# Optimization experiments

Hardware: AMD Instinct MI355X
Metric: run time of the kernel (lower is better)

## Reference

```python
import jax, jax.numpy as jnp
import numpy as np

B = 32768
IN_FULL = 3 * 32 * 32   # 3072 flattened
IN_DIM = 1024           # capped input dim
EMBED = 16
TINY = 16               # max(16, hidden_dim//4) with hidden_dim=32
OUT = 1000
NE = 4


def setup_inputs() -> dict:
    key = jax.random.key(0)
    ks = jax.random.split(key, 10)
    s = 0.05
    return {
        "x": jax.random.normal(ks[0], (B, 3, 32, 32), dtype=jnp.float32),
        "W_embed": jax.random.normal(ks[1], (EMBED, IN_DIM), dtype=jnp.float32) * s,
        "b_embed": jax.random.normal(ks[2], (EMBED,), dtype=jnp.float32) * s,
        "W1": jax.random.normal(ks[3], (NE, EMBED, TINY), dtype=jnp.float32) * s,
        "b1": jax.random.normal(ks[4], (NE, TINY), dtype=jnp.float32) * s,
        "W2": jax.random.normal(ks[5], (NE, TINY, OUT), dtype=jnp.float32) * s,
        "b2": jax.random.normal(ks[6], (NE, OUT), dtype=jnp.float32) * s,
        "Wg": jax.random.normal(ks[7], (NE, EMBED), dtype=jnp.float32) * s,
        "bg": jax.random.normal(ks[8], (NE,), dtype=jnp.float32) * s,
    }


def reference(x, W_embed, b_embed, W1, b1, W2, b2, Wg, bg):
    # flatten and truncate to input_dim (torch: x.view(B,-1)[:, :1024])
    xf = x.reshape(x.shape[0], -1)[:, :IN_DIM]
    # shared embedding: relu(Linear)
    e = jax.nn.relu(xf @ W_embed.T + b_embed)              # [B, EMBED]
    # gate: softmax(Linear)
    gate = jax.nn.softmax(e @ Wg.T + bg, axis=-1)          # [B, NE]
    # all 4 experts batched: relu(fc1) -> fc2 (dropout is eval-mode identity)
    h = jax.nn.relu(jnp.einsum('bd,edh->beh', e, W1) + b1[None])   # [B, NE, TINY]
    eo = jnp.einsum('beh,eho->beo', h, W2) + b2[None]              # [B, NE, OUT]
    # gate-weighted sum over experts
    out = jnp.einsum('beo,be->bo', eo, gate)               # [B, OUT]
    return out
```

## Files before the change

### kernel.cpp

```cpp
#include <hip/hip_runtime.h>
#include <cstddef>
#include <cstdint>

typedef short short8 __attribute__((ext_vector_type(8)));
typedef float floatx4 __attribute__((ext_vector_type(4)));

#define BATCH   32768
#define IN_DIM  1024
#define ROW_F   3072
#define EMBED   16
#define TINY    16
#define OUT     1000
#define NE      4
#define KPAD    96
#define NT_N    63

#define HW_BYTES ((size_t)BATCH * KPAD * 2)
#define BF_BYTES ((size_t)NT_N * 3 * 64 * 8 * 2)
#define WEF_SHORTS (32 * 64 * 8 * 2)

__device__ __forceinline__ unsigned short f2bf_rne(float f) {
    unsigned u = __builtin_bit_cast(unsigned, f);
    return (unsigned short)((u + 0x7FFFu + ((u >> 16) & 1u)) >> 16);
}

__global__ void k_prep(const float* __restrict__ W2, const float* __restrict__ b2,
                       const float* __restrict__ W_embed,
                       unsigned short* __restrict__ Bf,
                       unsigned short* __restrict__ WeF) {
    int tid = blockIdx.x * 256 + threadIdx.x;
    if (blockIdx.x < 48) {
        if (tid >= NT_N * 3 * 64) return;
        int n = tid / 192, r = tid % 192, s = r / 64, lane = r % 64;
        int col = n * 16 + (lane & 15);
        int kq = s * 32 + (lane >> 4) * 8;
        #pragma unroll
        for (int i = 0; i < 8; ++i) {
            int k = kq + i;
            float v = 0.f;
            if (col < OUT) {
                if (k < 64) v = W2[(size_t)((k >> 4) * 16 + (k & 15)) * OUT + col];
                else if (k < 68) v = b2[(size_t)(k - 64) * OUT + col];
            }
            Bf[(size_t)tid * 8 + i] = f2bf_rne(v);
        }
    } else {
        int id = tid - 48 * 256;
        if (id >= 32 * 64) return;
        int s = id >> 6, lane = id & 63;
        int j = lane & 15;
        int kq = s * 32 + ((lane >> 4) << 3);
        #pragma unroll
        for (int i = 0; i < 8; ++i) {
            float w = W_embed[(size_t)j * IN_DIM + kq + i];
            unsigned u = __builtin_bit_cast(unsigned, w);
            WeF[id * 8 + i] = (unsigned short)(u >> 16);
            float hif = __builtin_bit_cast(float, u & 0xFFFF0000u);
            float d = w - hif;
            WeF[16384 + id * 8 + i] =
                (unsigned short)(__builtin_bit_cast(unsigned, d) >> 16);
        }
    }
}

__global__ __launch_bounds__(256, 2) void k_embed(
    const float* __restrict__ x, const unsigned short* __restrict__ WeF,
    const float* __restrict__ b_embed, const float* __restrict__ W1,
    const float* __restrict__ b1, const float* __restrict__ Wg,
    const float* __restrict__ bg, unsigned short* __restrict__ hw)
{
    __shared__ short bb_lds[WEF_SHORTS];
    __shared__ float e_lds[4][16 * 20];
    __shared__ float g_lds[4][64];

    const int tid = threadIdx.x;
    {
        const float4* src = (const float4*)WeF;
        float4* dst = (float4*)bb_lds;
        #pragma unroll
        for (int i = 0; i < 16; ++i)
            dst[tid + i * 256] = src[tid + i * 256];
    }
    __syncthreads();

    const int lane = tid & 63;
    const int wv   = tid >> 6;
    const int quad = lane >> 4;
    const int jcol = lane & 15;
    const int tile = blockIdx.x * 4 + wv;
    const int row0 = tile * 16;

    const float be  = b_embed[jcol];
    const float bgr = bg[quad];
    float wgr[EMBED], w1r[EMBED];
    #pragma unroll
    for (int j = 0; j < EMBED; ++j) {
        wgr[j] = Wg[quad * EMBED + j];
        w1r[j] = W1[(size_t)(quad * EMBED + j) * TINY + jcol];
    }
    const float b1r = b1[lane];

    const short8* bhv = (const short8*)bb_lds;
    const short8* blv = (const short8*)(bb_lds + 16384);

    const float* xrow = x + (size_t)(row0 + jcol) * ROW_F + quad * 8;

    floatx4 acc0 = {0, 0, 0, 0}, acc1 = {0, 0, 0, 0};

    auto step = [&](float4 A0, float4 A1, int s) {
        float fa[8] = {A0.x, A0.y, A0.z, A0.w, A1.x, A1.y, A1.z, A1.w};
        short8 ahi, alo;
        #pragma unroll
        for (int m = 0; m < 8; ++m) {
            unsigned u = __builtin_bit_cast(unsigned, fa[m]);
            ahi[m] = (short)(u >> 16);
            float hif = __builtin_bit_cast(float, u & 0xFFFF0000u);
            float d = fa[m] - hif;
            alo[m] = (short)(__builtin_bit_cast(unsigned, d) >> 16);
        }
        short8 bh = bhv[s * 64 + lane];
        short8 bl = blv[s * 64 + lane];
        acc0 = __builtin_amdgcn_mfma_f32_16x16x32_bf16(ahi, bh, acc0, 0, 0, 0);
        acc1 = __builtin_amdgcn_mfma_f32_16x16x32_bf16(ahi, bl, acc1, 0, 0, 0);
        acc1 = __builtin_amdgcn_mfma_f32_16x16x32_bf16(alo, bh, acc1, 0, 0, 0);
    };

    float4 c0, c1, c2, c3, n0, n1, n2, n3;
    c0 = *(const float4*)(xrow + 0);
    c1 = *(const float4*)(xrow + 4);
    c2 = *(const float4*)(xrow + 32);
    c3 = *(const float4*)(xrow + 36);
    #pragma unroll
    for (int sp = 0; sp < 16; ++sp) {
        if (sp < 15) {
            const float* p = xrow + (sp * 2 + 2) * 32;
            n0 = *(const float4*)(p + 0);
            n1 = *(const float4*)(p + 4);
            n2 = *(const float4*)(p + 32);
            n3 = *(const float4*)(p + 36);
        }
        step(c0, c1, 2 * sp);
        step(c2, c3, 2 * sp + 1);
        c0 = n0; c1 = n1; c2 = n2; c3 = n3;
    }

    float* el = e_lds[wv];
    #pragma unroll
    for (int reg = 0; reg < 4; ++reg) {
        float e = fmaxf(acc0[reg] + acc1[reg] + be, 0.f);
        el[(quad * 4 + reg) * 20 + jcol] = e;
    }
    __syncthreads();

    {
        const int grow = lane & 15;
        float logit = bgr;
        #pragma unroll
        for (int j = 0; j < EMBED; ++j)
            logit = fmaf(el[grow * 20 + j], wgr[j], logit);
        float mx = fmaxf(logit, __shfl_xor(logit, 16));
        mx = fmaxf(mx, __shfl_xor(mx, 32));
        float ex = __expf(logit - mx);
        float sm = ex + __shfl_xor(ex, 16);
        sm = sm + __shfl_xor(sm, 32);
        g_lds[wv][lane] = ex / sm;
    }
    __syncthreads();

    #pragma unroll
    for (int r = 0; r < 16; ++r) {
        const float4* ev = (const float4*)(el + r * 20);
        float4 e0 = ev[0], e1 = ev[1], e2 = ev[2], e3 = ev[3];
        float h = b1r;
        h = fmaf(e0.x, w1r[0],  h); h = fmaf(e0.y, w1r[1],  h);
        h = fmaf(e0.z, w1r[2],  h); h = fmaf(e0.w, w1r[3],  h);
        h = fmaf(e1.x, w1r[4],  h); h = fmaf(e1.y, w1r[5],  h);
        h = fmaf(e1.z, w1r[6],  h); h = fmaf(e1.w, w1r[7],  h);
        h = fmaf(e2.x, w1r[8],  h); h = fmaf(e2.y, w1r[9],  h);
        h = fmaf(e2.z, w1r[10], h); h = fmaf(e2.w, w1r[11], h);
        h = fmaf(e3.x, w1r[12], h); h = fmaf(e3.y, w1r[13], h);
        h = fmaf(e3.z, w1r[14], h); h = fmaf(e3.w, w1r[15], h);
        h = fmaxf(h, 0.f);
        const float gate = g_lds[wv][quad * 16 + r];
        unsigned short* orow = hw + (size_t)(row0 + r) * KPAD;
        orow[lane] = f2bf_rne(gate * h);
        if (lane < 4)        orow[64 + lane] = f2bf_rne(g_lds[wv][lane * 16 + r]);
        else if (lane < 32)  orow[64 + lane] = 0;
    }
}

__global__ __launch_bounds__(256, 2) void k_out(
    const unsigned short* __restrict__ hw, const unsigned short* __restrict__ Bf,
    float* __restrict__ out)
{
    const int tid  = threadIdx.x;
    const int lane = tid & 63;
    const int wid  = blockIdx.x * 4 + (tid >> 6);
    const int g      = wid & 7;
    const int mstart = wid >> 3;
    const int nt0    = g * 8;
    const int NT     = (g == 7) ? 7 : 8;
    const int quad   = lane >> 4;
    const int cl     = lane & 15;

    const short8* bfv = (const short8*)Bf;
    const short8* hv  = (const short8*)hw;

    short8 bfrag[8][3];
    #pragma unroll
    for (int nt = 0; nt < 8; ++nt)
        if (nt < NT)
            #pragma unroll
            for (int s = 0; s < 3; ++s)
                bfrag[nt][s] = bfv[(size_t)((nt0 + nt) * 3 + s) * 64 + lane];

    int m = mstart;
    short8 a_cur[3], a_nxt[3];
    #pragma unroll
    for (int s = 0; s < 3; ++s)
        a_cur[s] = hv[(size_t)(m * 16 + cl) * 12 + s * 4 + quad];

    for (int t = 0; t < 8; ++t) {
        const int mn = m + 256;
        if (t < 7) {
            #pragma unroll
            for (int s = 0; s < 3; ++s)
                a_nxt[s] = hv[(size_t)(mn * 16 + cl) * 12 + s * 4 + quad];
        }

        floatx4 acc[8];
        #pragma unroll
        for (int nt = 0; nt < 8; ++nt) acc[nt] = (floatx4){0, 0, 0, 0};

        #pragma unroll
        for (int s = 0; s < 3; ++s)
            #pragma unroll
            for (int nt = 0; nt < 8; ++nt)
                if (nt < NT)
                    acc[nt] = __builtin_amdgcn_mfma_f32_16x16x32_bf16(
                        a_cur[s], bfrag[nt][s], acc[nt], 0, 0, 0);

        const int rowb = m * 16 + quad * 4;
        #pragma unroll
        for (int nt = 0; nt < 8; ++nt) {
            if (nt < NT) {
                const int col = (nt0 + nt) * 16 + cl;
                if (col < OUT) {
                    #pragma unroll
                    for (int reg = 0; reg < 4; ++reg)
                        out[(size_t)(rowb + reg) * OUT + col] = acc[nt][reg];
                }
            }
        }
        m = mn;
        #pragma unroll
        for (int s = 0; s < 3; ++s) a_cur[s] = a_nxt[s];
    }
}

extern "C" void kernel_launch(void* const* d_in, const int* in_sizes, int n_in,
                              void* d_out, int out_size, void* d_ws, size_t ws_size,
                              hipStream_t stream) {
    const float* x       = (const float*)d_in[0];
    const float* W_embed = (const float*)d_in[1];
    const float* b_embed = (const float*)d_in[2];
    const float* W1      = (const float*)d_in[3];
    const float* b1      = (const float*)d_in[4];
    const float* W2      = (const float*)d_in[5];
    const float* b2      = (const float*)d_in[6];
    const float* Wg      = (const float*)d_in[7];
    const float* bg      = (const float*)d_in[8];
    float* out = (float*)d_out;

    unsigned short* hw  = (unsigned short*)d_ws;
    unsigned short* Bf  = (unsigned short*)((char*)d_ws + HW_BYTES);
    unsigned short* WeF = (unsigned short*)((char*)d_ws + HW_BYTES + BF_BYTES);

    k_prep<<<56, 256, 0, stream>>>(W2, b2, W_embed, Bf, WeF);
    k_embed<<<512, 256, 0, stream>>>(x, WeF, b_embed, W1, b1, Wg, bg, hw);
    k_out<<<512, 256, 0, stream>>>(hw, Bf, out);
}
```

Baseline: 543.5 us.

## Fuse embed and output kernels, staging hidden tile in LDS

Merges the embedding/gate kernel and the output GEMM kernel into one 512-thread block kernel. The gated hidden activations now go to shared memory instead of a global workspace, so the hw round trip and one launch go away. The embed weight fragments are now read from global memory with register prefetch instead of being copied into LDS. In exchange, each wave's output GEMM waits behind a block-wide barrier, and the grid is 256 blocks, which may lower occupancy and overlap.

```diff
diff --git a/kernel.cpp b/kernel.cpp
--- a/kernel.cpp
+++ b/kernel.cpp
@@ -12,12 +12,10 @@
 #define TINY    16
 #define OUT     1000
 #define NE      4
-#define KPAD    96
 #define NT_N    63
-
-#define HW_BYTES ((size_t)BATCH * KPAD * 2)
+#define LSTR    104
+
 #define BF_BYTES ((size_t)NT_N * 3 * 64 * 8 * 2)
-#define WEF_SHORTS (32 * 64 * 8 * 2)
 
 __device__ __forceinline__ unsigned short f2bf_rne(float f) {
     unsigned u = __builtin_bit_cast(unsigned, f);
@@ -63,32 +61,23 @@
     }
 }
 
-__global__ __launch_bounds__(256, 2) void k_embed(
+__global__ __launch_bounds__(512, 2) void k_fused(
     const float* __restrict__ x, const unsigned short* __restrict__ WeF,
     const float* __restrict__ b_embed, const float* __restrict__ W1,
     const float* __restrict__ b1, const float* __restrict__ Wg,
-    const float* __restrict__ bg, unsigned short* __restrict__ hw)
+    const float* __restrict__ bg, const unsigned short* __restrict__ Bf,
+    float* __restrict__ out)
 {
-    __shared__ short bb_lds[WEF_SHORTS];
-    __shared__ float e_lds[4][16 * 20];
-    __shared__ float g_lds[4][64];
-
-    const int tid = threadIdx.x;
-    {
-        const float4* src = (const float4*)WeF;
-        float4* dst = (float4*)bb_lds;
-        #pragma unroll
-        for (int i = 0; i < 16; ++i)
-            dst[tid + i * 256] = src[tid + i * 256];
-    }
-    __syncthreads();
-
+    __shared__ float e_lds[8][16 * 20];
+    __shared__ float g_lds[8][64];
+    __shared__ __align__(16) short hwt[8][16][LSTR];
+
+    const int tid  = threadIdx.x;
     const int lane = tid & 63;
     const int wv   = tid >> 6;
     const int quad = lane >> 4;
     const int jcol = lane & 15;
-    const int tile = blockIdx.x * 4 + wv;
-    const int row0 = tile * 16;
+    const int row0 = (blockIdx.x * 8 + wv) * 16;
 
     const float be  = b_embed[jcol];
     const float bgr = bg[quad];
@@ -100,14 +89,14 @@
     }
     const float b1r = b1[lane];
 
-    const short8* bhv = (const short8*)bb_lds;
-    const short8* blv = (const short8*)(bb_lds + 16384);
+    const short8* bhv = (const short8*)WeF;
+    const short8* blv = bhv + 2048;
 
     const float* xrow = x + (size_t)(row0 + jcol) * ROW_F + quad * 8;
 
     floatx4 acc0 = {0, 0, 0, 0}, acc1 = {0, 0, 0, 0};
 
-    auto step = [&](float4 A0, float4 A1, int s) {
+    auto step = [&](float4 A0, float4 A1, short8 bh, short8 bl) {
         float fa[8] = {A0.x, A0.y, A0.z, A0.w, A1.x, A1.y, A1.z, A1.w};
         short8 ahi, alo;
         #pragma unroll
@@ -118,30 +107,36 @@
             float d = fa[m] - hif;
             alo[m] = (short)(__builtin_bit_cast(unsigned, d) >> 16);
         }
-        short8 bh = bhv[s * 64 + lane];
-        short8 bl = blv[s * 64 + lane];
         acc0 = __builtin_amdgcn_mfma_f32_16x16x32_bf16(ahi, bh, acc0, 0, 0, 0);
         acc1 = __builtin_amdgcn_mfma_f32_16x16x32_bf16(ahi, bl, acc1, 0, 0, 0);
         acc1 = __builtin_amdgcn_mfma_f32_16x16x32_bf16(alo, bh, acc1, 0, 0, 0);
     };
 
     float4 c0, c1, c2, c3, n0, n1, n2, n3;
+    short8 wh0 = bhv[lane],      wl0 = blv[lane];
+    short8 wh1 = bhv[64 + lane], wl1 = blv[64 + lane];
     c0 = *(const float4*)(xrow + 0);
     c1 = *(const float4*)(xrow + 4);
     c2 = *(const float4*)(xrow + 32);
     c3 = *(const float4*)(xrow + 36);
     #pragma unroll
     for (int sp = 0; sp < 16; ++sp) {
+        short8 nh0 = wh0, nl0 = wl0, nh1 = wh1, nl1 = wl1;
         if (sp < 15) {
             const float* p = xrow + (sp * 2 + 2) * 32;
             n0 = *(const float4*)(p + 0);
             n1 = *(const float4*)(p + 4);
             n2 = *(const float4*)(p + 32);
             n3 = *(const float4*)(p + 36);
-        }
-        step(c0, c1, 2 * sp);
-        step(c2, c3, 2 * sp + 1);
+            nh0 = bhv[(2 * sp + 2) * 64 + lane];
+            nl0 = blv[(2 * sp + 2) * 64 + lane];
+            nh1 = bhv[(2 * sp + 3) * 64 + lane];
+            nl1 = blv[(2 * sp + 3) * 64 + lane];
+        }
+        step(c0, c1, wh0, wl0);
+        step(c2, c3, wh1, wl1);
         c0 = n0; c1 = n1; c2 = n2; c3 = n3;
+        wh0 = nh0; wl0 = nl0; wh1 = nh1; wl1 = nl1;
     }
 
     float* el = e_lds[wv];
@@ -182,29 +177,16 @@
         h = fmaf(e3.z, w1r[14], h); h = fmaf(e3.w, w1r[15], h);
         h = fmaxf(h, 0.f);
         const float gate = g_lds[wv][quad * 16 + r];
-        unsigned short* orow = hw + (size_t)(row0 + r) * KPAD;
-        orow[lane] = f2bf_rne(gate * h);
-        if (lane < 4)        orow[64 + lane] = f2bf_rne(g_lds[wv][lane * 16 + r]);
+        short* orow = hwt[wv][r];
+        orow[lane] = (short)f2bf_rne(gate * h);
+        if (lane < 4)        orow[64 + lane] = (short)f2bf_rne(g_lds[wv][lane * 16 + r]);
         else if (lane < 32)  orow[64 + lane] = 0;
     }
-}
-
-__global__ __launch_bounds__(256, 2) void k_out(
-    const unsigned short* __restrict__ hw, const unsigned short* __restrict__ Bf,
-    float* __restrict__ out)
-{
-    const int tid  = threadIdx.x;
-    const int lane = tid & 63;
-    const int wid  = blockIdx.x * 4 + (tid >> 6);
-    const int g      = wid & 7;
-    const int mstart = wid >> 3;
-    const int nt0    = g * 8;
-    const int NT     = (g == 7) ? 7 : 8;
-    const int quad   = lane >> 4;
-    const int cl     = lane & 15;
-
+
+    const int nt0 = wv * 8;
+    const int NT  = (wv == 7) ? 7 : 8;
+    const int cl  = lane & 15;
     const short8* bfv = (const short8*)Bf;
-    const short8* hv  = (const short8*)hw;
 
     short8 bfrag[8][3];
     #pragma unroll
@@ -214,33 +196,32 @@
             for (int s = 0; s < 3; ++s)
                 bfrag[nt][s] = bfv[(size_t)((nt0 + nt) * 3 + s) * 64 + lane];
 
-    int m = mstart;
-    short8 a_cur[3], a_nxt[3];
-    #pragma unroll
-    for (int s = 0; s < 3; ++s)
-        a_cur[s] = hv[(size_t)(m * 16 + cl) * 12 + s * 4 + quad];
-
-    for (int t = 0; t < 8; ++t) {
-        const int mn = m + 256;
-        if (t < 7) {
-            #pragma unroll
-            for (int s = 0; s < 3; ++s)
-                a_nxt[s] = hv[(size_t)(mn * 16 + cl) * 12 + s * 4 + quad];
-        }
+    __syncthreads();
+
+    for (int mt = 0; mt < 8; ++mt) {
+        const short* arow = hwt[mt][cl];
+        short8 a0 = *(const short8*)(arow + (0 * 4 + quad) * 8);
+        short8 a1 = *(const short8*)(arow + (1 * 4 + quad) * 8);
+        short8 a2 = *(const short8*)(arow + (2 * 4 + quad) * 8);
 
         floatx4 acc[8];
         #pragma unroll
         for (int nt = 0; nt < 8; ++nt) acc[nt] = (floatx4){0, 0, 0, 0};
 
         #pragma unroll
-        for (int s = 0; s < 3; ++s)
-            #pragma unroll
-            for (int nt = 0; nt < 8; ++nt)
-                if (nt < NT)
-                    acc[nt] = __builtin_amdgcn_mfma_f32_16x16x32_bf16(
-                        a_cur[s], bfrag[nt][s], acc[nt], 0, 0, 0);
-
-        const int rowb = m * 16 + quad * 4;
+        for (int nt = 0; nt < 8; ++nt)
+            if (nt < NT)
+                acc[nt] = __builtin_amdgcn_mfma_f32_16x16x32_bf16(a0, bfrag[nt][0], acc[nt], 0, 0, 0);
+        #pragma unroll
+        for (int nt = 0; nt < 8; ++nt)
+            if (nt < NT)
+                acc[nt] = __builtin_amdgcn_mfma_f32_16x16x32_bf16(a1, bfrag[nt][1], acc[nt], 0, 0, 0);
+        #pragma unroll
+        for (int nt = 0; nt < 8; ++nt)
+            if (nt < NT)
+                acc[nt] = __builtin_amdgcn_mfma_f32_16x16x32_bf16(a2, bfrag[nt][2], acc[nt], 0, 0, 0);
+
+        const int rowb = (blockIdx.x * 8 + mt) * 16 + quad * 4;
         #pragma unroll
         for (int nt = 0; nt < 8; ++nt) {
             if (nt < NT) {
@@ -252,9 +233,6 @@
                 }
             }
         }
-        m = mn;
-        #pragma unroll
-        for (int s = 0; s < 3; ++s) a_cur[s] = a_nxt[s];
     }
 }
 
@@ -272,11 +250,9 @@
     const float* bg      = (const float*)d_in[8];
     float* out = (float*)d_out;
 
-    unsigned short* hw  = (unsigned short*)d_ws;
-    unsigned short* Bf  = (unsigned short*)((char*)d_ws + HW_BYTES);
-    unsigned short* WeF = (unsigned short*)((char*)d_ws + HW_BYTES + BF_BYTES);
+    unsigned short* Bf  = (unsigned short*)d_ws;
+    unsigned short* WeF = (unsigned short*)((char*)d_ws + BF_BYTES);
 
     k_prep<<<56, 256, 0, stream>>>(W2, b2, W_embed, Bf, WeF);
-    k_embed<<<512, 256, 0, stream>>>(x, WeF, b_embed, W1, b1, Wg, bg, hw);
-    k_out<<<512, 256, 0, stream>>>(hw, Bf, out);
-}
+    k_fused<<<256, 512, 0, stream>>>(x, WeF, b_embed, W1, b1, Wg, bg, Bf, out);
+}
```

Result: faster. 532.2 us (-2.1%).
